# Kernel optimization log

Hardware: AMD Instinct MI355X
Metric: run time of the kernel (lower is better)

## Reference

```python
import jax, jax.numpy as jnp
import numpy as np

B, M, C, S, SD, K, H = 32, 448, 384, 512, 128, 8, 8
DH = C // H
EPS = 1e-5
NEG_SLOPE = 0.2


def setup_inputs() -> dict:
    key = jax.random.key(0)
    ks = iter(jax.random.split(key, 32))
    nrm = lambda shape, scale=0.05: (jax.random.normal(next(ks), shape, jnp.float32) * scale)
    inp = {
        'q': jax.random.normal(next(ks), (B, M, C), jnp.float32),
        'coarse': jax.random.normal(next(ks), (B, M, 3), jnp.float32),
        'skeleton': jax.random.normal(next(ks), (B, S, 3), jnp.float32),
        # GraphConv 1: 3 -> 64 (root weight, rel/neighbor weight, bias)
        'gc1_wroot': nrm((3, 64), 0.3), 'gc1_wrel': nrm((3, 64), 0.3), 'gc1_b': jnp.zeros((64,), jnp.float32),
        # GraphConv 2: 64 -> SD
        'gc2_wroot': nrm((64, SD), 0.1), 'gc2_wrel': nrm((64, SD), 0.1), 'gc2_b': jnp.zeros((SD,), jnp.float32),
        # skeleton_projection: SD -> C
        'proj_w': nrm((SD, C), 0.08), 'proj_b': jnp.zeros((C,), jnp.float32),
        # MultiheadAttention (torch layout: in_proj (3C, C), out_proj (C, C))
        'attn_in_w': nrm((3 * C, C), 0.05), 'attn_in_b': jnp.zeros((3 * C,), jnp.float32),
        'attn_out_w': nrm((C, C), 0.05), 'attn_out_b': jnp.zeros((C,), jnp.float32),
        # increase_dim: Conv1d(C,1024,1) + BN(1024) + LeakyReLU + Conv1d(1024,1024,1)
        'inc1_w': nrm((1024, C), 0.05), 'inc1_b': jnp.zeros((1024,), jnp.float32),
        'bn_g': jnp.ones((1024,), jnp.float32), 'bn_b': jnp.zeros((1024,), jnp.float32),
        'bn_m': jnp.zeros((1024,), jnp.float32), 'bn_v': jnp.ones((1024,), jnp.float32),
        'inc2_w': nrm((1024, 1024), 0.03), 'inc2_b': jnp.zeros((1024,), jnp.float32),
        # reduce_map: Linear(C + 1024 + 3, C)
        'red_w': nrm((1024 + C + 3, C), 0.03), 'red_b': jnp.zeros((C,), jnp.float32),
    }
    return inp


def _knn_idx(pts):
    # pts: [B,S,3]; per-batch kNN (self excluded), matching knn_graph(k=K, batch=...)
    d2 = jnp.sum((pts[:, :, None, :] - pts[:, None, :, :]) ** 2, axis=-1)  # [B,S,S]
    d2 = d2 + jnp.eye(S, dtype=pts.dtype)[None] * 1e10                       # mask self
    _, idx = jax.lax.top_k(-d2, K)                                           # [B,S,K]
    return idx


def _graph_conv(x, idx, wroot, wrel, b):
    # GraphConv (PyG, aggr='add'): out_i = x_i Wroot + (sum_{j in N(i)} x_j) Wrel + b
    nb = jax.vmap(lambda f, i: f[i])(x, idx)   # [B,S,K,F]
    agg = nb.sum(axis=2)                       # [B,S,F]
    return x @ wroot + agg @ wrel + b


def reference(q, coarse, skeleton, gc1_wroot, gc1_wrel, gc1_b, gc2_wroot, gc2_wrel, gc2_b,
              proj_w, proj_b, attn_in_w, attn_in_b, attn_out_w, attn_out_b,
              inc1_w, inc1_b, bn_g, bn_b, bn_m, bn_v, inc2_w, inc2_b, red_w, red_b):
    # --- skeleton branch: knn graph + 2-layer GraphConv + max-pool + projection ---
    idx = _knn_idx(skeleton)
    h = _graph_conv(skeleton, idx, gc1_wroot, gc1_wrel, gc1_b)
    h = jax.nn.relu(h)
    h = _graph_conv(h, idx, gc2_wroot, gc2_wrel, gc2_b)        # [B,S,SD]
    proxy = jnp.max(h, axis=1)                                  # [B,SD]
    proxy = proxy @ proj_w + proj_b                             # [B,C]
    kv = jnp.broadcast_to(proxy[:, None, :], (B, M, C))         # expanded proxies

    # --- cross attention (torch nn.MultiheadAttention math) ---
    wq, wk, wv = attn_in_w[:C], attn_in_w[C:2 * C], attn_in_w[2 * C:]
    bq, bk, bv = attn_in_b[:C], attn_in_b[C:2 * C], attn_in_b[2 * C:]
    qh = (q @ wq.T + bq).reshape(B, M, H, DH)
    kh = (kv @ wk.T + bk).reshape(B, M, H, DH)
    vh = (kv @ wv.T + bv).reshape(B, M, H, DH)
    scores = jnp.einsum('bmhd,bnhd->bhmn', qh, kh) / jnp.sqrt(jnp.float32(DH))
    attn = jax.nn.softmax(scores, axis=-1)
    ctx = jnp.einsum('bhmn,bnhd->bmhd', attn, vh).reshape(B, M, C)
    q = ctx @ attn_out_w.T + attn_out_b                         # fused features [B,M,C]

    # --- increase_dim (1x1 conv == matmul) + BN(eval) + LeakyReLU + 1x1 conv ---
    g = jnp.einsum('bmc,oc->bmo', q, inc1_w) + inc1_b           # [B,M,1024]
    g = bn_g * (g - bn_m) * jax.lax.rsqrt(bn_v + EPS) + bn_b
    g = jnp.where(g >= 0, g, NEG_SLOPE * g)
    g = jnp.einsum('bmc,oc->bmo', g, inc2_w) + inc2_b
    global_feature = jnp.max(g, axis=1)                         # [B,1024]

    # --- concat + reduce_map ---
    rebuild = jnp.concatenate([jnp.broadcast_to(global_feature[:, None, :], (B, M, 1024)), q, coarse], axis=-1)
    out = rebuild @ red_w + red_b                               # [B,M,C]
    return out
```

## Files before the change

### kernel.cpp

```cpp
#include <hip/hip_runtime.h>

#define NB 32
#define MM 448
#define CC 384
#define SS 512
#define KNN 8

#define WS_IDX   0u
#define WS_H1    524288u
#define WS_PMAX  (WS_H1 + 4194304u)
#define WS_Q     (WS_PMAX + 262144u)
#define WS_Y     (WS_Q + 49152u)
#define WS_G2    (WS_Y + 131072u)
#define WS_PP    WS_H1
#define WS_VV    WS_IDX

__global__ __launch_bounds__(256) void k_knn_gc1(
    const float* __restrict__ skel,
    const float* __restrict__ w1root, const float* __restrict__ w1rel,
    const float* __restrict__ b1,
    int* __restrict__ idx_ws, float* __restrict__ h1_ws)
{
  int b   = blockIdx.x >> 7;
  int grp = blockIdx.x & 127;
  __shared__ __align__(16) float4 sk[SS];
  const float* sb = skel + b * SS * 3;
  for (int t = threadIdx.x; t < SS; t += 256)
    sk[t] = make_float4(sb[t*3+0], sb[t*3+1], sb[t*3+2], 0.f);
  __syncthreads();

  int wave = threadIdx.x >> 6, lane = threadIdx.x & 63;
  int i = grp * 4 + wave;
  float4 pi = sk[i];

  float bd[KNN];
#pragma unroll
  for (int t = 0; t < KNN; t++) {
    int j = lane + (t << 6);
    float4 p = sk[j];
    float d2;
    {
#pragma clang fp contract(off)
      float dx = pi.x - p.x, dy = pi.y - p.y, dz = pi.z - p.z;
      d2 = (dx*dx + dy*dy) + dz*dz;
    }
    bd[t] = (j == i) ? 3e38f : d2;
  }

  int win[KNN];
  int* idx_base = idx_ws + (size_t)(b*SS + i) * KNN;
#pragma unroll
  for (int t = 0; t < KNN; t++) {
    float bestd = bd[0]; int bests = 0;
#pragma unroll
    for (int s = 1; s < KNN; s++)
      if (bd[s] < bestd) { bestd = bd[s]; bests = s; }
    int bestj = lane + (bests << 6);
#pragma unroll
    for (int m = 1; m < 64; m <<= 1) {
      float od = __shfl_xor(bestd, m, 64);
      int   oj = __shfl_xor(bestj, m, 64);
      if (od < bestd || (od == bestd && oj < bestj)) { bestd = od; bestj = oj; }
    }
    win[t] = bestj;
    if (lane == t) idx_base[t] = bestj;
    if ((bestj & 63) == lane) {
      int sl = bestj >> 6;
#pragma unroll
      for (int s = 0; s < KNN; s++) if (s == sl) bd[s] = 3e38f;
    }
  }

  float a0 = 0.f, a1 = 0.f, a2 = 0.f;
#pragma unroll
  for (int t = 0; t < KNN; t++) {
    float4 n = sk[win[t]];
    a0 += n.x; a1 += n.y; a2 += n.z;
  }

  int c = lane;
  float h = b1[c] + pi.x*w1root[c] + pi.y*w1root[64+c] + pi.z*w1root[128+c]
                  + a0*w1rel[c]   + a1*w1rel[64+c]   + a2*w1rel[128+c];
  h = fmaxf(h, 0.f);
  h1_ws[(size_t)(b*SS + i) * 64 + lane] = h;
}

__global__ __launch_bounds__(256) void k_gc2_max(
    const float* __restrict__ h1_ws, const int* __restrict__ idx_ws,
    const float* __restrict__ w2root, const float* __restrict__ w2rel,
    const float* __restrict__ b2, float* __restrict__ pmax)
{
  int b = blockIdx.x >> 4, chunk = blockIdx.x & 15;
  int r0 = chunk * 32;
  __shared__ __align__(16) float X[32*129];
  __shared__ __align__(16) float Wt[32*128];
  __shared__ float mred[8*128];
  __shared__ int nbs[32*KNN];

  const float* h1b = h1_ws + (size_t)b * SS * 64;
  nbs[threadIdx.x] = idx_ws[(b*SS + r0)*KNN + threadIdx.x];
#pragma unroll
  for (int p = 0; p < 8; p++) {
    int idx = threadIdx.x + 256*p;
    int r = idx >> 6, k = idx & 63;
    X[r*129 + k] = h1b[(r0 + r)*64 + k];
  }
  __syncthreads();
#pragma unroll
  for (int p = 0; p < 8; p++) {
    int idx = threadIdx.x + 256*p;
    int r = idx >> 6, k = idx & 63;
    const int* nb = nbs + r*KNN;
    float s = 0.f;
#pragma unroll
    for (int j = 0; j < KNN; j++) s += h1b[nb[j]*64 + k];
    X[r*129 + 64 + k] = s;
  }

  int rg = threadIdx.x >> 5, cg = threadIdx.x & 31;
  float acc[4][4];
#pragma unroll
  for (int r = 0; r < 4; r++)
#pragma unroll
    for (int u = 0; u < 4; u++) acc[r][u] = 0.f;

  const float* wsrc[4] = { w2root, w2root + 32*128, w2rel, w2rel + 32*128 };
#pragma unroll 1
  for (int ch = 0; ch < 4; ch++) {
    __syncthreads();
    const float* ws = wsrc[ch];
#pragma unroll
    for (int p = 0; p < 16; p++) {
      int idx = threadIdx.x + 256*p;
      Wt[idx] = ws[idx];
    }
    __syncthreads();
    int kb = ch * 32;
    const float* xr0 = X + (rg*4+0)*129 + kb;
    const float* xr1 = X + (rg*4+1)*129 + kb;
    const float* xr2 = X + (rg*4+2)*129 + kb;
    const float* xr3 = X + (rg*4+3)*129 + kb;
#pragma unroll 4
    for (int k = 0; k < 32; k++) {
      float4 w4 = *(const float4*)(Wt + k*128 + cg*4);
      float x0 = xr0[k], x1 = xr1[k], x2 = xr2[k], x3 = xr3[k];
      acc[0][0] += x0*w4.x; acc[0][1] += x0*w4.y; acc[0][2] += x0*w4.z; acc[0][3] += x0*w4.w;
      acc[1][0] += x1*w4.x; acc[1][1] += x1*w4.y; acc[1][2] += x1*w4.z; acc[1][3] += x1*w4.w;
      acc[2][0] += x2*w4.x; acc[2][1] += x2*w4.y; acc[2][2] += x2*w4.z; acc[2][3] += x2*w4.w;
      acc[3][0] += x3*w4.x; acc[3][1] += x3*w4.y; acc[3][2] += x3*w4.z; acc[3][3] += x3*w4.w;
    }
  }
#pragma unroll
  for (int u = 0; u < 4; u++)
    mred[rg*128 + cg*4 + u] =
      fmaxf(fmaxf(acc[0][u], acc[1][u]), fmaxf(acc[2][u], acc[3][u]));
  __syncthreads();
  if (threadIdx.x < 128) {
    int col = threadIdx.x;
    float mx = mred[col];
#pragma unroll
    for (int g = 1; g < 8; g++) mx = fmaxf(mx, mred[g*128 + col]);
    pmax[(size_t)(b*16 + chunk)*128 + col] = mx + b2[col];
  }
}

__global__ __launch_bounds__(256) void k_chainA(
    const float* __restrict__ pmax,
    const float* __restrict__ projw, const float* __restrict__ projb,
    const float* __restrict__ aiw, const float* __restrict__ aib,
    float* __restrict__ vv_ws)
{
  int b = blockIdx.x / 12, sl = blockIdx.x % 12;
  int t = threadIdx.x;
  __shared__ __align__(16) float proxy[128];
  __shared__ __align__(16) float kv[CC];
  if (t < 128) {
    float m = -3e38f;
    for (int ch = 0; ch < 16; ch++)
      m = fmaxf(m, pmax[(size_t)(b*16 + ch)*128 + t]);
    proxy[t] = m;
  }
  __syncthreads();
  for (int c = t; c < CC; c += 256) {
    float acc = projb[c];
    for (int s = 0; s < 128; s++) acc += proxy[s] * projw[s*CC + c];
    kv[c] = acc;
  }
  __syncthreads();
  int o = sl*32 + (t >> 3), qq = t & 7;
  const float* wr = aiw + (size_t)(2*CC + o) * CC + qq*48;
  const float* xr = kv + qq*48;
  float acc = 0.f;
#pragma unroll
  for (int k = 0; k < 48; k += 4) {
    float4 w4 = *(const float4*)(wr + k);
    float4 x4 = *(const float4*)(xr + k);
    acc += w4.x*x4.x + w4.y*x4.y + w4.z*x4.z + w4.w*x4.w;
  }
  acc += __shfl_xor(acc, 1, 64);
  acc += __shfl_xor(acc, 2, 64);
  acc += __shfl_xor(acc, 4, 64);
  if (qq == 0) vv_ws[b*CC + o] = acc + aib[2*CC + o];
}

__global__ __launch_bounds__(256) void k_chainB(
    const float* __restrict__ vv_ws,
    const float* __restrict__ aow, const float* __restrict__ aob,
    const float* __restrict__ i1w, const float* __restrict__ i1b,
    const float* __restrict__ bng, const float* __restrict__ bnb,
    const float* __restrict__ bnm, const float* __restrict__ bnv,
    float* __restrict__ q_ws, float* __restrict__ y_ws)
{
  int b = blockIdx.x >> 3, sl = blockIdx.x & 7;
  int t = threadIdx.x;
  __shared__ __align__(16) float vv[CC];
  __shared__ __align__(16) float qv[CC];
  for (int i = t; i < CC; i += 256) vv[i] = vv_ws[b*CC + i];
  __syncthreads();
  {
    int qq = t & 3;
    const float* xr = vv + qq*96;
#pragma unroll 1
    for (int r = 0; r < 6; r++) {
      int o = r*64 + (t >> 2);
      const float* wr = aow + (size_t)o * CC + qq*96;
      float acc = 0.f;
#pragma unroll
      for (int k = 0; k < 96; k += 4) {
        float4 w4 = *(const float4*)(wr + k);
        float4 x4 = *(const float4*)(xr + k);
        acc += w4.x*x4.x + w4.y*x4.y + w4.z*x4.z + w4.w*x4.w;
      }
      acc += __shfl_xor(acc, 1, 64);
      acc += __shfl_xor(acc, 2, 64);
      if (qq == 0) {
        float v = acc + aob[o];
        qv[o] = v;
        if (sl == 0) q_ws[b*CC + o] = v;
      }
    }
  }
  __syncthreads();
  {
    int o = sl*128 + (t >> 1), qq = t & 1;
    const float* wr = i1w + (size_t)o * CC + qq*192;
    const float* xr = qv + qq*192;
    float acc = 0.f;
#pragma unroll 12
    for (int k = 0; k < 192; k += 4) {
      float4 w4 = *(const float4*)(wr + k);
      float4 x4 = *(const float4*)(xr + k);
      acc += w4.x*x4.x + w4.y*x4.y + w4.z*x4.z + w4.w*x4.w;
    }
    acc += __shfl_xor(acc, 1, 64);
    if (qq == 0) {
      float a = acc + i1b[o];
      float z = bng[o] * (a - bnm[o]) * rsqrtf(bnv[o] + 1e-5f) + bnb[o];
      y_ws[b*1024 + o] = (z >= 0.f) ? z : 0.2f * z;
    }
  }
}

__global__ __launch_bounds__(256) void k_inc2(
    const float* __restrict__ y_ws, const float* __restrict__ inc2_w,
    const float* __restrict__ inc2_b, float* __restrict__ g2_ws)
{
  int b = blockIdx.x >> 4, og = blockIdx.x & 15;
  int t = threadIdx.x;
  int o = og*64 + (t >> 2), qq = t & 3;
  __shared__ __align__(16) float xs[1024];
  for (int i = t; i < 1024; i += 256) xs[i] = y_ws[b*1024 + i];
  __syncthreads();
  const float* wr = inc2_w + (size_t)o * 1024 + qq*256;
  const float* xr = xs + qq*256;
  float acc = 0.f;
#pragma unroll 8
  for (int kk = 0; kk < 256; kk += 4) {
    float4 w4 = *(const float4*)(wr + kk);
    float4 x4 = *(const float4*)(xr + kk);
    acc += w4.x*x4.x + w4.y*x4.y + w4.z*x4.z + w4.w*x4.w;
  }
  acc += __shfl_xor(acc, 1, 64);
  acc += __shfl_xor(acc, 2, 64);
  if (qq == 0) g2_ws[b*1024 + o] = acc + inc2_b[o];
}

__global__ __launch_bounds__(256) void k_basep(
    const float* __restrict__ g2_ws, const float* __restrict__ q_ws,
    const float* __restrict__ red_w, float* __restrict__ pp)
{
  int cg = blockIdx.x;
  int o0 = blockIdx.y * 64;
  int c0 = cg * 32;
  __shared__ __align__(16) float xs[32*33];
  __shared__ __align__(16) float wt[32*64];
#pragma unroll
  for (int p = 0; p < 8; p++) {
    int idx = threadIdx.x + 256*p;
    int c = idx >> 6, o = idx & 63;
    wt[idx] = red_w[(size_t)(c0 + c)*CC + o0 + o];
  }
  {
    int b = threadIdx.x >> 3, cp = threadIdx.x & 7;
    const float* src = (cg < 32) ? (g2_ws + b*1024 + c0)
                                 : (q_ws  + b*CC   + (c0 - 1024));
    float4 v = *(const float4*)(src + cp*4);
    xs[(cp*4+0)*33 + b] = v.x;
    xs[(cp*4+1)*33 + b] = v.y;
    xs[(cp*4+2)*33 + b] = v.z;
    xs[(cp*4+3)*33 + b] = v.w;
  }
  __syncthreads();
  int b = threadIdx.x >> 3, og = threadIdx.x & 7;
  float acc[8];
#pragma unroll
  for (int u = 0; u < 8; u++) acc[u] = 0.f;
#pragma unroll 8
  for (int c = 0; c < 32; c++) {
    float xv = xs[c*33 + b];
    float4 w0 = *(const float4*)(wt + c*64 + og*8);
    float4 w1 = *(const float4*)(wt + c*64 + og*8 + 4);
    acc[0] += xv*w0.x; acc[1] += xv*w0.y; acc[2] += xv*w0.z; acc[3] += xv*w0.w;
    acc[4] += xv*w1.x; acc[5] += xv*w1.y; acc[6] += xv*w1.z; acc[7] += xv*w1.w;
  }
  float* dst = pp + (size_t)(cg*32 + b)*CC + o0 + og*8;
  *(float4*)dst       = make_float4(acc[0], acc[1], acc[2], acc[3]);
  *(float4*)(dst + 4) = make_float4(acc[4], acc[5], acc[6], acc[7]);
}

__global__ __launch_bounds__(256) void k_out2(
    const float* __restrict__ pp, const float* __restrict__ red_b,
    const float* __restrict__ red_w, const float* __restrict__ coarse,
    float* __restrict__ out)
{
  int b = blockIdx.x, mc = blockIdx.y;
  int t = threadIdx.x;
  __shared__ __align__(16) float baseS[CC];
  __shared__ __align__(16) float w3[3*CC];
  __shared__ float crs[32*4];
  for (int c = t; c < CC; c += 256) {
    float s = red_b[c];
#pragma unroll 4
    for (int cg = 0; cg < 44; cg++) s += pp[(size_t)cg*12288 + b*CC + c];
    baseS[c] = s;
  }
  for (int i = t; i < 3*CC; i += 256) w3[i] = red_w[(size_t)1408*CC + i];
  if (t < 96) {
    int r = t / 3, j = t % 3;
    crs[r*4 + j] = coarse[(size_t)(b*MM + mc*32 + r)*3 + j];
  }
  __syncthreads();
  int m0 = mc * 32;
#pragma unroll 4
  for (int p = 0; p < 12; p++) {
    int idx = t + 256*p;
    int r = idx / 96, c4 = idx % 96;
    int c = c4 * 4;
    float4 b4 = *(const float4*)(baseS + c);
    float4 w0 = *(const float4*)(w3 + c);
    float4 w1 = *(const float4*)(w3 + CC + c);
    float4 w2 = *(const float4*)(w3 + 2*CC + c);
    float cx = crs[r*4+0], cy = crs[r*4+1], cz = crs[r*4+2];
    float4 o4;
    o4.x = b4.x + cx*w0.x + cy*w1.x + cz*w2.x;
    o4.y = b4.y + cx*w0.y + cy*w1.y + cz*w2.y;
    o4.z = b4.z + cx*w0.z + cy*w1.z + cz*w2.z;
    o4.w = b4.w + cx*w0.w + cy*w1.w + cz*w2.w;
    *(float4*)(out + (size_t)(b*MM + m0 + r)*CC + c) = o4;
  }
}

extern "C" void kernel_launch(void* const* d_in, const int* in_sizes, int n_in,
                              void* d_out, int out_size, void* d_ws, size_t ws_size,
                              hipStream_t stream)
{
  (void)in_sizes; (void)n_in; (void)out_size; (void)ws_size;
  const float* coarse = (const float*)d_in[1];
  const float* skel   = (const float*)d_in[2];
  const float* g1wr   = (const float*)d_in[3];
  const float* g1wl   = (const float*)d_in[4];
  const float* g1b    = (const float*)d_in[5];
  const float* g2wr   = (const float*)d_in[6];
  const float* g2wl   = (const float*)d_in[7];
  const float* g2b    = (const float*)d_in[8];
  const float* projw  = (const float*)d_in[9];
  const float* projb  = (const float*)d_in[10];
  const float* aiw    = (const float*)d_in[11];
  const float* aib    = (const float*)d_in[12];
  const float* aow    = (const float*)d_in[13];
  const float* aob    = (const float*)d_in[14];
  const float* i1w    = (const float*)d_in[15];
  const float* i1b    = (const float*)d_in[16];
  const float* bng    = (const float*)d_in[17];
  const float* bnb    = (const float*)d_in[18];
  const float* bnm    = (const float*)d_in[19];
  const float* bnv    = (const float*)d_in[20];
  const float* i2w    = (const float*)d_in[21];
  const float* i2b    = (const float*)d_in[22];
  const float* redw   = (const float*)d_in[23];
  const float* redb   = (const float*)d_in[24];
  float* out = (float*)d_out;

  char* ws = (char*)d_ws;
  int*   idx_ws = (int*)(ws + WS_IDX);
  float* h1_ws  = (float*)(ws + WS_H1);
  float* pmax   = (float*)(ws + WS_PMAX);
  float* q_ws   = (float*)(ws + WS_Q);
  float* y_ws   = (float*)(ws + WS_Y);
  float* g2_ws  = (float*)(ws + WS_G2);
  float* pp     = (float*)(ws + WS_PP);
  float* vv_ws  = (float*)(ws + WS_VV);

  k_knn_gc1<<<4096, 256, 0, stream>>>(skel, g1wr, g1wl, g1b, idx_ws, h1_ws);
  k_gc2_max<<<512, 256, 0, stream>>>(h1_ws, idx_ws, g2wr, g2wl, g2b, pmax);
  k_chainA<<<384, 256, 0, stream>>>(pmax, projw, projb, aiw, aib, vv_ws);
  k_chainB<<<256, 256, 0, stream>>>(vv_ws, aow, aob, i1w, i1b,
                                    bng, bnb, bnm, bnv, q_ws, y_ws);
  k_inc2<<<512, 256, 0, stream>>>(y_ws, i2w, i2b, g2_ws);
  k_basep<<<dim3(44, 6), 256, 0, stream>>>(g2_ws, q_ws, redw, pp);
  k_out2<<<dim3(32, 14), 256, 0, stream>>>(pp, redb, redw, coarse, out);
}
```

Before: 247.1 us.

## Tile inc2 GEMV as split-K batched GEMM with partials reduced in basep

The inc2 matvec previously read the full 4MB weight matrix once per batch element, 32 times in total. It is now a batched GEMM tiled over 64-wide output and K chunks, so each weight tile is loaded once and reused across all 32 batch rows through shared memory. Split-K partial sums go to a new workspace region, and basep adds them up together with the bias. This trades a small extra partial buffer and reduction work for far less weight traffic.

```diff
diff --git a/kernel.cpp b/kernel.cpp
--- a/kernel.cpp
+++ b/kernel.cpp
@@ -11,9 +11,9 @@
 #define WS_PMAX  (WS_H1 + 4194304u)
 #define WS_Q     (WS_PMAX + 262144u)
 #define WS_Y     (WS_Q + 49152u)
-#define WS_G2    (WS_Y + 131072u)
 #define WS_PP    WS_H1
 #define WS_VV    WS_IDX
+#define WS_G2P   8388608u
 
 __global__ __launch_bounds__(256) void k_knn_gc1(
     const float* __restrict__ skel,
@@ -262,31 +262,47 @@
 }
 
 __global__ __launch_bounds__(256) void k_inc2(
-    const float* __restrict__ y_ws, const float* __restrict__ inc2_w,
-    const float* __restrict__ inc2_b, float* __restrict__ g2_ws)
-{
-  int b = blockIdx.x >> 4, og = blockIdx.x & 15;
+    const float* __restrict__ y_ws, const float* __restrict__ i2w,
+    float* __restrict__ g2p)
+{
+  int kc = blockIdx.x, oc = blockIdx.y;
   int t = threadIdx.x;
-  int o = og*64 + (t >> 2), qq = t & 3;
-  __shared__ __align__(16) float xs[1024];
-  for (int i = t; i < 1024; i += 256) xs[i] = y_ws[b*1024 + i];
-  __syncthreads();
-  const float* wr = inc2_w + (size_t)o * 1024 + qq*256;
-  const float* xr = xs + qq*256;
-  float acc = 0.f;
-#pragma unroll 8
-  for (int kk = 0; kk < 256; kk += 4) {
-    float4 w4 = *(const float4*)(wr + kk);
-    float4 x4 = *(const float4*)(xr + kk);
-    acc += w4.x*x4.x + w4.y*x4.y + w4.z*x4.z + w4.w*x4.w;
-  }
-  acc += __shfl_xor(acc, 1, 64);
-  acc += __shfl_xor(acc, 2, 64);
-  if (qq == 0) g2_ws[b*1024 + o] = acc + inc2_b[o];
+  __shared__ __align__(16) float ys[32*64];
+  __shared__ __align__(16) float wt[64*65];
+#pragma unroll
+  for (int p = 0; p < 8; p++) {
+    int idx = t + 256*p;
+    int b = idx >> 6, k = idx & 63;
+    ys[idx] = y_ws[b*1024 + kc*64 + k];
+  }
+#pragma unroll
+  for (int p = 0; p < 16; p++) {
+    int idx = t + 256*p;
+    int o = idx >> 6, k = idx & 63;
+    wt[k*65 + o] = i2w[(size_t)(oc*64 + o)*1024 + kc*64 + k];
+  }
+  __syncthreads();
+  int b = t >> 3, og = t & 7;
+  float acc[8];
+#pragma unroll
+  for (int u = 0; u < 8; u++) acc[u] = 0.f;
+  const float* yb = ys + b*64;
+#pragma unroll 4
+  for (int k = 0; k < 64; k++) {
+    float yv = yb[k];
+    float4 w0 = *(const float4*)(wt + k*65 + og*8);
+    float4 w1 = *(const float4*)(wt + k*65 + og*8 + 4);
+    acc[0] += yv*w0.x; acc[1] += yv*w0.y; acc[2] += yv*w0.z; acc[3] += yv*w0.w;
+    acc[4] += yv*w1.x; acc[5] += yv*w1.y; acc[6] += yv*w1.z; acc[7] += yv*w1.w;
+  }
+  float* dst = g2p + (size_t)(kc*32 + b)*1024 + oc*64 + og*8;
+  *(float4*)dst       = make_float4(acc[0], acc[1], acc[2], acc[3]);
+  *(float4*)(dst + 4) = make_float4(acc[4], acc[5], acc[6], acc[7]);
 }
 
 __global__ __launch_bounds__(256) void k_basep(
-    const float* __restrict__ g2_ws, const float* __restrict__ q_ws,
+    const float* __restrict__ g2p, const float* __restrict__ i2b,
+    const float* __restrict__ q_ws,
     const float* __restrict__ red_w, float* __restrict__ pp)
 {
   int cg = blockIdx.x;
@@ -302,13 +318,27 @@
   }
   {
     int b = threadIdx.x >> 3, cp = threadIdx.x & 7;
-    const float* src = (cg < 32) ? (g2_ws + b*1024 + c0)
-                                 : (q_ws  + b*CC   + (c0 - 1024));
-    float4 v = *(const float4*)(src + cp*4);
-    xs[(cp*4+0)*33 + b] = v.x;
-    xs[(cp*4+1)*33 + b] = v.y;
-    xs[(cp*4+2)*33 + b] = v.z;
-    xs[(cp*4+3)*33 + b] = v.w;
+    if (cg < 32) {
+      float4 s;
+      const float* pb = g2p + b*1024 + c0 + cp*4;
+      s.x = i2b[c0+cp*4+0]; s.y = i2b[c0+cp*4+1];
+      s.z = i2b[c0+cp*4+2]; s.w = i2b[c0+cp*4+3];
+#pragma unroll 4
+      for (int kp = 0; kp < 16; kp++) {
+        float4 v = *(const float4*)(pb + (size_t)kp*32768);
+        s.x += v.x; s.y += v.y; s.z += v.z; s.w += v.w;
+      }
+      xs[(cp*4+0)*33 + b] = s.x;
+      xs[(cp*4+1)*33 + b] = s.y;
+      xs[(cp*4+2)*33 + b] = s.z;
+      xs[(cp*4+3)*33 + b] = s.w;
+    } else {
+      float4 v = *(const float4*)(q_ws + b*CC + (c0 - 1024) + cp*4);
+      xs[(cp*4+0)*33 + b] = v.x;
+      xs[(cp*4+1)*33 + b] = v.y;
+      xs[(cp*4+2)*33 + b] = v.z;
+      xs[(cp*4+3)*33 + b] = v.w;
+    }
   }
   __syncthreads();
   int b = threadIdx.x >> 3, og = threadIdx.x & 7;
@@ -407,16 +437,16 @@
   float* pmax   = (float*)(ws + WS_PMAX);
   float* q_ws   = (float*)(ws + WS_Q);
   float* y_ws   = (float*)(ws + WS_Y);
-  float* g2_ws  = (float*)(ws + WS_G2);
   float* pp     = (float*)(ws + WS_PP);
   float* vv_ws  = (float*)(ws + WS_VV);
+  float* g2p    = (float*)(ws + WS_G2P);
 
   k_knn_gc1<<<4096, 256, 0, stream>>>(skel, g1wr, g1wl, g1b, idx_ws, h1_ws);
   k_gc2_max<<<512, 256, 0, stream>>>(h1_ws, idx_ws, g2wr, g2wl, g2b, pmax);
   k_chainA<<<384, 256, 0, stream>>>(pmax, projw, projb, aiw, aib, vv_ws);
   k_chainB<<<256, 256, 0, stream>>>(vv_ws, aow, aob, i1w, i1b,
                                     bng, bnb, bnm, bnv, q_ws, y_ws);
-  k_inc2<<<512, 256, 0, stream>>>(y_ws, i2w, i2b, g2_ws);
-  k_basep<<<dim3(44, 6), 256, 0, stream>>>(g2_ws, q_ws, redw, pp);
+  k_inc2<<<dim3(16, 16), 256, 0, stream>>>(y_ws, i2w, g2p);
+  k_basep<<<dim3(44, 6), 256, 0, stream>>>(g2p, i2b, q_ws, redw, pp);
   k_out2<<<dim3(32, 14), 256, 0, stream>>>(pp, redb, redw, coarse, out);
 }
```

Result: faster. 235.3 us (-4.8%).
